# Kernel tuning notes

Measured on AMD Instinct MI355X. Metric: run time of the kernel, lower is better.

Reference implementation:

```python
import jax, jax.numpy as jnp
import numpy as np

H, KVH, HD = 32, 8, 128          # query heads, kv heads, head_dim
HIDDEN = H * HD                   # 4096
TOTAL_KV = 3072                   # sum of (start_pos + seqlen) over the batch (static)
ROPE_THETA = 10000.0


def setup_inputs() -> dict:
    key = jax.random.key(0)
    ks = jax.random.split(key, 4)
    x = jax.random.normal(ks[0], (1024, HIDDEN), jnp.float32)
    wqkv = jax.random.normal(ks[1], (HIDDEN, HIDDEN + 2 * KVH * HD), jnp.float32) * 0.02
    wo = jax.random.normal(ks[2], (HIDDEN, HIDDEN), jnp.float32) * 0.02
    # paged cache: [num_layers=1, 2(k/v), cache_slots, kv_heads, head_dim], holds post-RoPE prefixes
    kv_cache = jax.random.normal(ks[3], (1, 2, 8192, KVH, HD), jnp.float32) * 0.02
    # 4 ragged requests: seqlens [512,256,128,128], cached prefixes [0,512,1024,512]
    seqstarts = jnp.array([0, 512, 768, 896, 1024], jnp.int32)
    start_pos = jnp.array([0, 512, 1024, 512], jnp.int32)
    kvstarts = jnp.array([0, 512, 1280, 2432, 3072], jnp.int32)  # cumsum of start_pos+seqlen
    cachestarts = jnp.array([0, 1024, 2560, 4096], jnp.int32)    # page base per request
    return dict(x=x, wqkv=wqkv, wo=wo, kv_cache=kv_cache, seqstarts=seqstarts,
                kvstarts=kvstarts, cachestarts=cachestarts, start_pos=start_pos)


def _rope(t, pos):
    # interleaved (GPT-J style) rotary over full head_dim; t: [T, nheads, HD], pos: [T]
    d2 = HD // 2
    inv_freq = 1.0 / (ROPE_THETA ** (jnp.arange(d2, dtype=jnp.float32) / d2))
    ang = pos.astype(jnp.float32)[:, None] * inv_freq      # [T, d2]
    cos = jnp.cos(ang)[:, None, :]
    sin = jnp.sin(ang)[:, None, :]
    x1, x2 = t[..., 0::2], t[..., 1::2]
    r1 = x1 * cos - x2 * sin
    r2 = x1 * sin + x2 * cos
    return jnp.stack([r1, r2], axis=-1).reshape(t.shape)


def _forward(x, wqkv, wo, kv_cache, seqstarts, kvstarts, cachestarts, start_pos):
    T = x.shape[0]
    # fused QKV projection
    xqkv = (x @ wqkv).reshape(T, H + 2 * KVH, HD)
    xq, xk, xv = jnp.split(xqkv, [H, H + KVH], axis=1)   # [T,32,HD],[T,8,HD],[T,8,HD]

    # per-token batch id and absolute position (ragged via seqstarts)
    tok = jnp.arange(T)
    bq = jnp.searchsorted(seqstarts, tok, side='right') - 1
    pos_q = tok - seqstarts[bq] + start_pos[bq]
    xq = _rope(xq, pos_q)
    xk = _rope(xk, pos_q)

    # assemble ragged KV stream: cached prefix (paged cache) + freshly projected tokens
    kvtok = jnp.arange(TOTAL_KV)
    bkv = jnp.searchsorted(kvstarts, kvtok, side='right') - 1
    pkv = kvtok - kvstarts[bkv]                              # absolute kv position
    is_new = pkv >= start_pos[bkv]
    new_idx = jnp.clip(seqstarts[bkv] + pkv - start_pos[bkv], 0, T - 1)
    cache_idx = cachestarts[bkv] + pkv                       # paged slot for prefix
    keys = jnp.where(is_new[:, None, None], xk[new_idx], kv_cache[0, 0][cache_idx])
    vals = jnp.where(is_new[:, None, None], xv[new_idx], kv_cache[0, 1][cache_idx])

    # GQA: repeat kv heads to match query heads
    rep = H // KVH
    keys = jnp.repeat(keys, rep, axis=1)                     # [TOTAL_KV, 32, HD]
    vals = jnp.repeat(vals, rep, axis=1)

    scale = 1.0 / jnp.sqrt(jnp.float32(HD))
    scores = jnp.einsum('qhd,khd->hqk', xq, keys) * scale    # [32, T, TOTAL_KV]
    # ragged causal mask: same request and kv position <= query position
    mask = (bq[:, None] == bkv[None, :]) & (pkv[None, :] <= pos_q[:, None])
    scores = jnp.where(mask[None], scores, jnp.float32(-1e30))
    probs = jax.nn.softmax(scores, axis=-1)
    attn = jnp.einsum('hqk,khd->qhd', probs, vals)           # [T, 32, HD]
    return attn.reshape(T, HIDDEN) @ wo


def reference(x, wqkv, wo, kv_cache, seqstarts, kvstarts, cachestarts, start_pos):
    return _forward(x, wqkv, wo, kv_cache, seqstarts, kvstarts, cachestarts, start_pos)
```

## Files before the change

kernel.cpp:

```cpp
#include <hip/hip_runtime.h>
#include <hip/hip_bf16.h>
#include <math.h>
#include <stdint.h>

typedef __bf16 bf16;
typedef __attribute__((ext_vector_type(4))) float floatx4;
typedef __attribute__((ext_vector_type(8))) bf16 bf16x8;
typedef __attribute__((ext_vector_type(4))) bf16 bf16x4;

#define LDS_ASYNC16(gptr, lptr)                                                \
  __builtin_amdgcn_global_load_lds(                                            \
      (const __attribute__((address_space(1))) void*)(gptr),                   \
      (__attribute__((address_space(3))) void*)(lptr), 16, 0, 0)

__global__ __launch_bounds__(256) void k_cvt(const float* __restrict__ in,
                                             bf16* __restrict__ out) {
  int i = (blockIdx.x * 256 + threadIdx.x) * 4;
  float4 v = *(const float4*)(in + i);
  bf16x4 o;
  o[0] = (bf16)v.x; o[1] = (bf16)v.y; o[2] = (bf16)v.z; o[3] = (bf16)v.w;
  *(bf16x4*)(out + i) = o;
}

__global__ __launch_bounds__(256) void k_transpose_cvt(const float* __restrict__ in,
                                                       bf16* __restrict__ out,
                                                       int K, int N) {
  __shared__ float tile[64][65];
  int k0 = blockIdx.y * 64, n0 = blockIdx.x * 64;
  int tid = threadIdx.x;
  int cg = tid & 15, rr = tid >> 4;
#pragma unroll
  for (int p = 0; p < 4; ++p) {
    int r = rr + p * 16;
    float4 v = *(const float4*)(in + (size_t)(k0 + r) * N + n0 + cg * 4);
    tile[r][cg * 4 + 0] = v.x; tile[r][cg * 4 + 1] = v.y;
    tile[r][cg * 4 + 2] = v.z; tile[r][cg * 4 + 3] = v.w;
  }
  __syncthreads();
#pragma unroll
  for (int p = 0; p < 4; ++p) {
    int n = rr + p * 16;
    bf16x4 o;
    o[0] = (bf16)tile[cg * 4 + 0][n];
    o[1] = (bf16)tile[cg * 4 + 1][n];
    o[2] = (bf16)tile[cg * 4 + 2][n];
    o[3] = (bf16)tile[cg * 4 + 3][n];
    *(bf16x4*)(out + (size_t)(n0 + n) * K + k0 + cg * 4) = o;
  }
}

__global__ __launch_bounds__(256) void k_gemm_bt(const bf16* __restrict__ A,
                                                 const bf16* __restrict__ B,
                                                 float* __restrict__ C,
                                                 int M, int N, int K) {
  __shared__ bf16 As[128 * 32];
  __shared__ bf16 Bs[128 * 32];
  int tid = threadIdx.x;
  int w = tid >> 6, lane = tid & 63;
  int lq = lane >> 4, l16 = lane & 15;
  int bm = blockIdx.y * 128, bn = blockIdx.x * 128;
  int wm = (w >> 1) * 64, wn = (w & 1) * 64;
  floatx4 acc[4][4] = {};
  const bf16* Ab = A + (size_t)bm * K;
  const bf16* Bb = B + (size_t)bn * K;
  int srow = (lane >> 2);
  int scol = (lane & 3) * 8;

  for (int k0 = 0; k0 < K; k0 += 32) {
#pragma unroll
    for (int c = 0; c < 2; ++c) {
      int r = w * 32 + c * 16 + srow;
      LDS_ASYNC16(Ab + (size_t)r * K + k0 + scol, &As[(w * 32 + c * 16) * 32]);
      LDS_ASYNC16(Bb + (size_t)r * K + k0 + scol, &Bs[(w * 32 + c * 16) * 32]);
    }
    __syncthreads();
    bf16x8 af[4], bfr[4];
#pragma unroll
    for (int i = 0; i < 4; ++i)
      af[i] = *(const bf16x8*)&As[(wm + i * 16 + l16) * 32 + lq * 8];
#pragma unroll
    for (int j = 0; j < 4; ++j)
      bfr[j] = *(const bf16x8*)&Bs[(wn + j * 16 + l16) * 32 + lq * 8];
#pragma unroll
    for (int i = 0; i < 4; ++i)
#pragma unroll
      for (int j = 0; j < 4; ++j)
        acc[i][j] = __builtin_amdgcn_mfma_f32_16x16x32_bf16(af[i], bfr[j],
                                                            acc[i][j], 0, 0, 0);
    __syncthreads();
  }
#pragma unroll
  for (int i = 0; i < 4; ++i)
#pragma unroll
    for (int j = 0; j < 4; ++j) {
      int m = bm + wm + i * 16 + lq * 4;
      int n = bn + wn + j * 16 + l16;
      float* cp = C + (size_t)m * N + n;
#pragma unroll
      for (int r = 0; r < 4; ++r) cp[(size_t)r * N] = acc[i][j][r];
    }
}

__global__ __launch_bounds__(256) void k_rope(const float* __restrict__ xqkv,
                                              bf16* __restrict__ qb,
                                              bf16* __restrict__ kb,
                                              const int* __restrict__ seqstarts,
                                              const int* __restrict__ start_pos) {
  int t = blockIdx.x;
  int s = 0;
  for (int i = 1; i < 4; ++i) if (seqstarts[i] <= t) s = i;
  float pos = (float)(t - seqstarts[s] + start_pos[s]);
  for (int wk = threadIdx.x; wk < 40 * 64; wk += 256) {
    int hh = wk >> 6, j = wk & 63;
    const float* src = xqkv + ((size_t)t * 48 + hh) * 128 + 2 * j;
    float x1 = src[0], x2 = src[1];
    float invf = exp2f(-(float)j * 0.20762050593045935f);
    float ang = pos * invf;
    float sv, cv;
    sincosf(ang, &sv, &cv);
    float r1 = x1 * cv - x2 * sv;
    float r2 = x1 * sv + x2 * cv;
    unsigned int u1 = (unsigned int)__builtin_bit_cast(unsigned short, (bf16)r1);
    unsigned int u2 = (unsigned int)__builtin_bit_cast(unsigned short, (bf16)r2);
    unsigned int pk = u1 | (u2 << 16);
    unsigned int* dst = (hh < 32)
        ? (unsigned int*)(qb + ((size_t)t * 32 + hh) * 128)
        : (unsigned int*)(kb + ((size_t)t * 8 + (hh - 32)) * 128);
    dst[j] = pk;
  }
}

__global__ __launch_bounds__(256) void k_assemble_k(
    const bf16* __restrict__ xk, const float* __restrict__ ck,
    bf16* __restrict__ kall,
    const int* __restrict__ seqstarts, const int* __restrict__ kvstarts,
    const int* __restrict__ cachestarts, const int* __restrict__ start_pos) {
  int p = blockIdx.x;
  int b = 0;
  for (int i = 1; i < 4; ++i) if (kvstarts[i] <= p) b = i;
  int pkv = p - kvstarts[b];
  int tid = threadIdx.x;
  int hk = tid >> 5, d4 = (tid & 31) * 4;
  bf16* dst = kall + ((size_t)hk * 3072 + p) * 128 + d4;
  if (pkv >= start_pos[b]) {
    int tn = seqstarts[b] + pkv - start_pos[b];
    *(bf16x4*)dst = *(const bf16x4*)(xk + ((size_t)tn * 8 + hk) * 128 + d4);
  } else {
    int ci = cachestarts[b] + pkv;
    float4 v = *(const float4*)(ck + ((size_t)ci * 8 + hk) * 128 + d4);
    bf16x4 o;
    o[0] = (bf16)v.x; o[1] = (bf16)v.y; o[2] = (bf16)v.z; o[3] = (bf16)v.w;
    *(bf16x4*)dst = o;
  }
}

__global__ __launch_bounds__(256) void k_assemble_vT(
    const float* __restrict__ xqkv, const float* __restrict__ cv,
    bf16* __restrict__ vT,
    const int* __restrict__ seqstarts, const int* __restrict__ kvstarts,
    const int* __restrict__ cachestarts, const int* __restrict__ start_pos) {
  __shared__ float tile[64][130];
  int hk = blockIdx.y, p0 = blockIdx.x * 64;
  int tid = threadIdx.x;
  {
    int r = tid >> 2;
    int p = p0 + r;
    int b = 0;
    for (int i = 1; i < 4; ++i) if (kvstarts[i] <= p) b = i;
    int pkv = p - kvstarts[b];
    const float* src;
    if (pkv >= start_pos[b]) {
      int tn = seqstarts[b] + pkv - start_pos[b];
      src = xqkv + (size_t)tn * 6144 + (40 + hk) * 128;
    } else {
      int ci = cachestarts[b] + pkv;
      src = cv + ((size_t)ci * 8 + hk) * 128;
    }
    int f0 = (tid & 3) * 32;
#pragma unroll
    for (int i = 0; i < 8; ++i) {
      float4 v = *(const float4*)(src + f0 + i * 4);
      tile[r][f0 + i * 4 + 0] = v.x; tile[r][f0 + i * 4 + 1] = v.y;
      tile[r][f0 + i * 4 + 2] = v.z; tile[r][f0 + i * 4 + 3] = v.w;
    }
  }
  __syncthreads();
  int d = tid >> 1, hf = tid & 1;
  bf16* dst = vT + ((size_t)hk * 128 + d) * 3072 + p0 + hf * 32;
#pragma unroll
  for (int q = 0; q < 4; ++q) {
    bf16x8 o;
#pragma unroll
    for (int e = 0; e < 8; ++e) o[e] = (bf16)tile[hf * 32 + q * 8 + e][d];
    *(bf16x8*)(dst + q * 8) = o;
  }
}

__global__ __launch_bounds__(256) void k_attn(
    const bf16* __restrict__ qb, const bf16* __restrict__ kall,
    const bf16* __restrict__ vT, bf16* __restrict__ aout,
    const int* __restrict__ seqstarts, const int* __restrict__ kvstarts,
    const int* __restrict__ start_pos) {
  __shared__ bf16 Qs[64 * 128];
  __shared__ bf16 Ks[64 * 128];
  __shared__ bf16 Vs[128 * 64];
  __shared__ bf16 Ps[64 * 64];
  int qbi = blockIdx.x, h = blockIdx.y, hk = h >> 2;
  int t0 = qbi * 64;
  int s = 0;
  for (int i = 1; i < 4; ++i) if (seqstarts[i] <= t0) s = i;
  int posbase = t0 - seqstarts[s] + start_pos[s];
  int kv0 = kvstarts[s];
  int nkv = posbase + 64;
  int tid = threadIdx.x, w = tid >> 6, lane = tid & 63;
  int lq = lane >> 4, l16 = lane & 15;

#pragma unroll
  for (int c = 0; c < 4; ++c) {
    int r = w * 16 + c * 4 + (lane >> 4);
    LDS_ASYNC16(qb + (((size_t)(t0 + r) * 32 + h) * 128 + (lane & 15) * 8),
                &Qs[(w * 16 + c * 4) * 128]);
  }
  float m_r[4], l_r[4];
  floatx4 oacc[8] = {};
#pragma unroll
  for (int rg = 0; rg < 4; ++rg) { m_r[rg] = -3.0e38f; l_r[rg] = 0.f; }
  const float scale = 0.08838834764831845f;

  for (int p0 = 0; p0 < nkv; p0 += 64) {
#pragma unroll
    for (int c = 0; c < 4; ++c) {
      int r = w * 16 + c * 4 + (lane >> 4);
      LDS_ASYNC16(kall + (((size_t)hk * 3072 + kv0 + p0 + r) * 128 + (lane & 15) * 8),
                  &Ks[(w * 16 + c * 4) * 128]);
    }
#pragma unroll
    for (int c = 0; c < 4; ++c) {
      int d = w * 32 + c * 8 + (lane >> 3);
      LDS_ASYNC16(vT + (((size_t)hk * 128 + d) * 3072 + kv0 + p0 + (lane & 7) * 8),
                  &Vs[(w * 32 + c * 8) * 64]);
    }
    __syncthreads();

    bf16x8 qa[4];
#pragma unroll
    for (int kk = 0; kk < 4; ++kk)
      qa[kk] = *(const bf16x8*)&Qs[(w * 16 + l16) * 128 + kk * 32 + lq * 8];
    floatx4 sacc[4] = {};
#pragma unroll
    for (int kk = 0; kk < 4; ++kk)
#pragma unroll
      for (int j = 0; j < 4; ++j) {
        bf16x8 kb = *(const bf16x8*)&Ks[(j * 16 + l16) * 128 + kk * 32 + lq * 8];
        sacc[j] = __builtin_amdgcn_mfma_f32_16x16x32_bf16(qa[kk], kb, sacc[j], 0, 0, 0);
      }

#pragma unroll
    for (int rg = 0; rg < 4; ++rg) {
      int qpos = posbase + w * 16 + lq * 4 + rg;
      float sv[4];
      float rmax = -3.0e38f;
#pragma unroll
      for (int j = 0; j < 4; ++j) {
        int pkv = p0 + j * 16 + l16;
        sv[j] = (pkv <= qpos) ? sacc[j][rg] * scale : -3.0e38f;
        rmax = fmaxf(rmax, sv[j]);
      }
#pragma unroll
      for (int off = 1; off < 16; off <<= 1)
        rmax = fmaxf(rmax, __shfl_xor(rmax, off, 64));
      float mnew = fmaxf(m_r[rg], rmax);
      float alpha = __expf(m_r[rg] - mnew);
      m_r[rg] = mnew;
      float psum = 0.f;
#pragma unroll
      for (int j = 0; j < 4; ++j) {
        float pv = __expf(sv[j] - mnew);
        psum += pv;
        Ps[(w * 16 + lq * 4 + rg) * 64 + j * 16 + l16] = (bf16)pv;
      }
#pragma unroll
      for (int off = 1; off < 16; off <<= 1) psum += __shfl_xor(psum, off, 64);
      l_r[rg] = l_r[rg] * alpha + psum;
#pragma unroll
      for (int nt = 0; nt < 8; ++nt) oacc[nt][rg] *= alpha;
    }

#pragma unroll
    for (int kk = 0; kk < 2; ++kk) {
      bf16x8 pa = *(const bf16x8*)&Ps[(w * 16 + l16) * 64 + kk * 32 + lq * 8];
#pragma unroll
      for (int nt = 0; nt < 8; ++nt) {
        bf16x8 vb = *(const bf16x8*)&Vs[(nt * 16 + l16) * 64 + kk * 32 + lq * 8];
        oacc[nt] = __builtin_amdgcn_mfma_f32_16x16x32_bf16(pa, vb, oacc[nt], 0, 0, 0);
      }
    }
    __syncthreads();
  }

#pragma unroll
  for (int rg = 0; rg < 4; ++rg) {
    float inv = 1.0f / l_r[rg];
    int t = t0 + w * 16 + lq * 4 + rg;
#pragma unroll
    for (int nt = 0; nt < 8; ++nt)
      aout[(size_t)t * 4096 + h * 128 + nt * 16 + l16] =
          (bf16)(oacc[nt][rg] * inv);
  }
}

extern "C" void kernel_launch(void* const* d_in, const int* in_sizes, int n_in,
                              void* d_out, int out_size, void* d_ws, size_t ws_size,
                              hipStream_t stream) {
  const float* x = (const float*)d_in[0];
  const float* wqkv = (const float*)d_in[1];
  const float* wo = (const float*)d_in[2];
  const float* kv = (const float*)d_in[3];
  const int* seqstarts = (const int*)d_in[4];
  const int* kvstarts = (const int*)d_in[5];
  const int* cachestarts = (const int*)d_in[6];
  const int* start_pos = (const int*)d_in[7];
  float* out = (float*)d_out;

  char* base = (char*)d_ws;
  size_t off = 0;
  auto carve = [&](size_t bytes) {
    void* r = base + off;
    off += (bytes + 255) & ~(size_t)255;
    return r;
  };
  bf16* x_bf    = (bf16*)carve(1024ull * 4096 * 2);
  bf16* wqkvT   = (bf16*)carve(6144ull * 4096 * 2);
  bf16* woT     = (bf16*)carve(4096ull * 4096 * 2);
  float* xqkv   = (float*)carve(1024ull * 6144 * 4);
  bf16* q_bf    = (bf16*)carve(1024ull * 32 * 128 * 2);
  bf16* xk_bf   = (bf16*)carve(1024ull * 8 * 128 * 2);
  bf16* k_all   = (bf16*)carve(8ull * 3072 * 128 * 2);
  bf16* vT_all  = (bf16*)carve(8ull * 128 * 3072 * 2);
  bf16* attn_bf = (bf16*)carve(1024ull * 4096 * 2);

  const float* cache_v = kv + 8192ull * 8 * 128;

  k_cvt<<<4096, 256, 0, stream>>>(x, x_bf);
  k_transpose_cvt<<<dim3(96, 64), 256, 0, stream>>>(wqkv, wqkvT, 4096, 6144);
  k_transpose_cvt<<<dim3(64, 64), 256, 0, stream>>>(wo, woT, 4096, 4096);
  k_gemm_bt<<<dim3(48, 8), 256, 0, stream>>>(x_bf, wqkvT, xqkv, 1024, 6144, 4096);
  k_rope<<<1024, 256, 0, stream>>>(xqkv, q_bf, xk_bf, seqstarts, start_pos);
  k_assemble_k<<<3072, 256, 0, stream>>>(xk_bf, kv, k_all, seqstarts, kvstarts,
                                         cachestarts, start_pos);
  k_assemble_vT<<<dim3(48, 8), 256, 0, stream>>>(xqkv, cache_v, vT_all, seqstarts,
                                                 kvstarts, cachestarts, start_pos);
  k_attn<<<dim3(16, 32), 256, 0, stream>>>(q_bf, k_all, vT_all, attn_bf,
                                           seqstarts, kvstarts, start_pos);
  k_gemm_bt<<<dim3(32, 8), 256, 0, stream>>>(attn_bf, woT, out, 1024, 4096, 4096);
}
```

Before: 550.2 us.

## Split-K both GEMMs by two and merge partial sums downstream

Both bf16 GEMMs now split the K dimension across two grid z-slices, each writing its own fp32 partial output. The QKV partials are summed inside the rope and V-assembly kernels, and the output projection partials are summed by a new elementwise merge kernel, reusing the dead wqkvT workspace. The aim is more blocks for better CU occupancy, since the grids were small relative to the CU count. The cost is extra fp32 partial writes and reads plus one added launch.

```diff
diff --git a/kernel.cpp b/kernel.cpp
--- a/kernel.cpp
+++ b/kernel.cpp
@@ -20,6 +20,17 @@
   bf16x4 o;
   o[0] = (bf16)v.x; o[1] = (bf16)v.y; o[2] = (bf16)v.z; o[3] = (bf16)v.w;
   *(bf16x4*)(out + i) = o;
+}
+
+__global__ __launch_bounds__(256) void k_merge(const float* __restrict__ a,
+                                               const float* __restrict__ b,
+                                               float* __restrict__ out) {
+  int i = (blockIdx.x * 256 + threadIdx.x) * 4;
+  float4 va = *(const float4*)(a + i);
+  float4 vb = *(const float4*)(b + i);
+  float4 o;
+  o.x = va.x + vb.x; o.y = va.y + vb.y; o.z = va.z + vb.z; o.w = va.w + vb.w;
+  *(float4*)(out + i) = o;
 }
 
 __global__ __launch_bounds__(256) void k_transpose_cvt(const float* __restrict__ in,
@@ -52,7 +63,7 @@
 __global__ __launch_bounds__(256) void k_gemm_bt(const bf16* __restrict__ A,
                                                  const bf16* __restrict__ B,
                                                  float* __restrict__ C,
-                                                 int M, int N, int K) {
+                                                 int M, int N, int K, int ksplit) {
   __shared__ bf16 As[128 * 32];
   __shared__ bf16 Bs[128 * 32];
   int tid = threadIdx.x;
@@ -60,13 +71,16 @@
   int lq = lane >> 4, l16 = lane & 15;
   int bm = blockIdx.y * 128, bn = blockIdx.x * 128;
   int wm = (w >> 1) * 64, wn = (w & 1) * 64;
+  int kc = K / ksplit;
+  int koff = blockIdx.z * kc;
+  C += (size_t)blockIdx.z * M * N;
   floatx4 acc[4][4] = {};
   const bf16* Ab = A + (size_t)bm * K;
   const bf16* Bb = B + (size_t)bn * K;
   int srow = (lane >> 2);
   int scol = (lane & 3) * 8;
 
-  for (int k0 = 0; k0 < K; k0 += 32) {
+  for (int k0 = koff; k0 < koff + kc; k0 += 32) {
 #pragma unroll
     for (int c = 0; c < 2; ++c) {
       int r = w * 32 + c * 16 + srow;
@@ -101,7 +115,8 @@
     }
 }
 
-__global__ __launch_bounds__(256) void k_rope(const float* __restrict__ xqkv,
+__global__ __launch_bounds__(256) void k_rope(const float* __restrict__ xp0,
+                                              const float* __restrict__ xp1,
                                               bf16* __restrict__ qb,
                                               bf16* __restrict__ kb,
                                               const int* __restrict__ seqstarts,
@@ -112,8 +127,9 @@
   float pos = (float)(t - seqstarts[s] + start_pos[s]);
   for (int wk = threadIdx.x; wk < 40 * 64; wk += 256) {
     int hh = wk >> 6, j = wk & 63;
-    const float* src = xqkv + ((size_t)t * 48 + hh) * 128 + 2 * j;
-    float x1 = src[0], x2 = src[1];
+    size_t idx = ((size_t)t * 48 + hh) * 128 + 2 * j;
+    float x1 = xp0[idx] + xp1[idx];
+    float x2 = xp0[idx + 1] + xp1[idx + 1];
     float invf = exp2f(-(float)j * 0.20762050593045935f);
     float ang = pos * invf;
     float sv, cv;
@@ -155,8 +171,8 @@
 }
 
 __global__ __launch_bounds__(256) void k_assemble_vT(
-    const float* __restrict__ xqkv, const float* __restrict__ cv,
-    bf16* __restrict__ vT,
+    const float* __restrict__ xp0, const float* __restrict__ xp1,
+    const float* __restrict__ cv, bf16* __restrict__ vT,
     const int* __restrict__ seqstarts, const int* __restrict__ kvstarts,
     const int* __restrict__ cachestarts, const int* __restrict__ start_pos) {
   __shared__ float tile[64][130];
@@ -168,20 +184,28 @@
     int b = 0;
     for (int i = 1; i < 4; ++i) if (kvstarts[i] <= p) b = i;
     int pkv = p - kvstarts[b];
-    const float* src;
+    int f0 = (tid & 3) * 32;
     if (pkv >= start_pos[b]) {
       int tn = seqstarts[b] + pkv - start_pos[b];
-      src = xqkv + (size_t)tn * 6144 + (40 + hk) * 128;
+      size_t base = (size_t)tn * 6144 + (40 + hk) * 128;
+#pragma unroll
+      for (int i = 0; i < 8; ++i) {
+        float4 v0 = *(const float4*)(xp0 + base + f0 + i * 4);
+        float4 v1 = *(const float4*)(xp1 + base + f0 + i * 4);
+        tile[r][f0 + i * 4 + 0] = v0.x + v1.x;
+        tile[r][f0 + i * 4 + 1] = v0.y + v1.y;
+        tile[r][f0 + i * 4 + 2] = v0.z + v1.z;
+        tile[r][f0 + i * 4 + 3] = v0.w + v1.w;
+      }
     } else {
       int ci = cachestarts[b] + pkv;
-      src = cv + ((size_t)ci * 8 + hk) * 128;
-    }
-    int f0 = (tid & 3) * 32;
-#pragma unroll
-    for (int i = 0; i < 8; ++i) {
-      float4 v = *(const float4*)(src + f0 + i * 4);
-      tile[r][f0 + i * 4 + 0] = v.x; tile[r][f0 + i * 4 + 1] = v.y;
-      tile[r][f0 + i * 4 + 2] = v.z; tile[r][f0 + i * 4 + 3] = v.w;
+      const float* src = cv + ((size_t)ci * 8 + hk) * 128;
+#pragma unroll
+      for (int i = 0; i < 8; ++i) {
+        float4 v = *(const float4*)(src + f0 + i * 4);
+        tile[r][f0 + i * 4 + 0] = v.x; tile[r][f0 + i * 4 + 1] = v.y;
+        tile[r][f0 + i * 4 + 2] = v.z; tile[r][f0 + i * 4 + 3] = v.w;
+      }
     }
   }
   __syncthreads();
@@ -332,25 +356,31 @@
   bf16* x_bf    = (bf16*)carve(1024ull * 4096 * 2);
   bf16* wqkvT   = (bf16*)carve(6144ull * 4096 * 2);
   bf16* woT     = (bf16*)carve(4096ull * 4096 * 2);
-  float* xqkv   = (float*)carve(1024ull * 6144 * 4);
+  float* xqkv   = (float*)carve(2ull * 1024 * 6144 * 4);
   bf16* q_bf    = (bf16*)carve(1024ull * 32 * 128 * 2);
   bf16* xk_bf   = (bf16*)carve(1024ull * 8 * 128 * 2);
   bf16* k_all   = (bf16*)carve(8ull * 3072 * 128 * 2);
   bf16* vT_all  = (bf16*)carve(8ull * 128 * 3072 * 2);
   bf16* attn_bf = (bf16*)carve(1024ull * 4096 * 2);
-
+  float* outp = (float*)wqkvT;
+
+  float* xqkv1 = xqkv + 1024ull * 6144;
   const float* cache_v = kv + 8192ull * 8 * 128;
 
   k_cvt<<<4096, 256, 0, stream>>>(x, x_bf);
   k_transpose_cvt<<<dim3(96, 64), 256, 0, stream>>>(wqkv, wqkvT, 4096, 6144);
   k_transpose_cvt<<<dim3(64, 64), 256, 0, stream>>>(wo, woT, 4096, 4096);
-  k_gemm_bt<<<dim3(48, 8), 256, 0, stream>>>(x_bf, wqkvT, xqkv, 1024, 6144, 4096);
-  k_rope<<<1024, 256, 0, stream>>>(xqkv, q_bf, xk_bf, seqstarts, start_pos);
+  k_gemm_bt<<<dim3(48, 8, 2), 256, 0, stream>>>(x_bf, wqkvT, xqkv, 1024, 6144,
+                                                4096, 2);
+  k_rope<<<1024, 256, 0, stream>>>(xqkv, xqkv1, q_bf, xk_bf, seqstarts, start_pos);
   k_assemble_k<<<3072, 256, 0, stream>>>(xk_bf, kv, k_all, seqstarts, kvstarts,
                                          cachestarts, start_pos);
-  k_assemble_vT<<<dim3(48, 8), 256, 0, stream>>>(xqkv, cache_v, vT_all, seqstarts,
-                                                 kvstarts, cachestarts, start_pos);
+  k_assemble_vT<<<dim3(48, 8), 256, 0, stream>>>(xqkv, xqkv1, cache_v, vT_all,
+                                                 seqstarts, kvstarts, cachestarts,
+                                                 start_pos);
   k_attn<<<dim3(16, 32), 256, 0, stream>>>(q_bf, k_all, vT_all, attn_bf,
                                            seqstarts, kvstarts, start_pos);
-  k_gemm_bt<<<dim3(32, 8), 256, 0, stream>>>(attn_bf, woT, out, 1024, 4096, 4096);
-}
+  k_gemm_bt<<<dim3(32, 8, 2), 256, 0, stream>>>(attn_bf, woT, outp, 1024, 4096,
+                                                4096, 2);
+  k_merge<<<4096, 256, 0, stream>>>(outp, outp + 1024ull * 4096, out);
+}
```

After: 507.1 us. 1.08x faster.
